# Performance work log

Hardware: AMD Instinct MI355X
Metric: run time of the kernel (lower is better)

The kernel has to match this reference:

```python
import jax, jax.numpy as jnp
import numpy as np

NUM_NODES = 100000
NUM_RELS = 50
NUM_BASES = 16
H_DIM = 16
OUT_DIM = 8
NUM_EDGES = 3200000


def setup_inputs() -> dict:
    key = jax.random.key(0)
    ks = jax.random.split(key, 10)
    inp = {
        "edge_src": jax.random.randint(ks[0], (NUM_EDGES,), 0, NUM_NODES, dtype=jnp.int32),
        "edge_dst": jax.random.randint(ks[1], (NUM_EDGES,), 0, NUM_NODES, dtype=jnp.int32),
        "edge_type": jax.random.randint(ks[2], (NUM_EDGES,), 0, NUM_RELS, dtype=jnp.int32),
        "edge_norm": jax.random.uniform(ks[3], (NUM_EDGES,), dtype=jnp.float32),
        "W0": jax.random.normal(ks[4], (NUM_BASES, NUM_NODES, H_DIM), dtype=jnp.float32) * 0.05,
        "C0": jax.random.normal(ks[5], (NUM_RELS, NUM_BASES), dtype=jnp.float32) * 0.05,
        "W1": jax.random.normal(ks[6], (NUM_BASES, H_DIM, H_DIM), dtype=jnp.float32) * 0.05,
        "C1": jax.random.normal(ks[7], (NUM_RELS, NUM_BASES), dtype=jnp.float32) * 0.05,
        "W2": jax.random.normal(ks[8], (NUM_BASES, H_DIM, OUT_DIM), dtype=jnp.float32) * 0.05,
        "C2": jax.random.normal(ks[9], (NUM_RELS, NUM_BASES), dtype=jnp.float32) * 0.05,
    }
    return inp


def _input_layer(src, dst, rel, norm, W0, C0):
    # basis combination: (R, N, h) embedding-per-relation table
    Wfull = jnp.einsum('rb,bnh->rnh', C0, W0)
    emb = Wfull.reshape(NUM_RELS * NUM_NODES, H_DIM)
    # per-edge gather by rel_type * in_feat + src_id, scaled by norm
    msg = emb[rel * NUM_NODES + src] * norm[:, None]
    h = jax.ops.segment_sum(msg, dst, num_segments=NUM_NODES)
    return jax.nn.relu(h)


def _dense_layer(h, src, dst, rel, norm, W, C, out_dim):
    # basis combination: (R, in, out)
    Wr = jnp.einsum('rb,bio->rio', C, W)
    # transform node features once per relation, then gather by (rel, src)
    Hr = jnp.einsum('ni,rio->rno', h, Wr)  # (R, N, out)
    msg = Hr[rel, src] * norm[:, None]     # (E, out)
    return jax.ops.segment_sum(msg, dst, num_segments=NUM_NODES)


def reference(edge_src, edge_dst, edge_type, edge_norm, W0, C0, W1, C1, W2, C2):
    h = _input_layer(edge_src, edge_dst, edge_type, edge_norm, W0, C0)
    h = jax.nn.relu(_dense_layer(h, edge_src, edge_dst, edge_type, edge_norm, W1, C1, H_DIM))
    h = jax.nn.softmax(_dense_layer(h, edge_src, edge_dst, edge_type, edge_norm, W2, C2, OUT_DIM), axis=1)
    return h
```

## Files before the change

### kernel.cpp

```cpp
#include <hip/hip_runtime.h>
#include <cstddef>
#include <cstdint>

#define E_TOTAL 3200000
#define N_NODES 100000
#define N_RELS 50
#define N_BASES 16
#define HD 16
#define OD 8
#define NTHR 256

#define NBKT 196
#define P1B 1024
#define P1C 3125
#define FP8_SCALE 256.0f
#define FP8_INV (1.0f / 256.0f)

typedef unsigned int u32;
typedef __attribute__((ext_vector_type(8))) short s16x8;
typedef __attribute__((ext_vector_type(4))) float f32x4;
typedef __attribute__((ext_vector_type(16))) float f32x16;

__device__ __forceinline__ u32 cvtpk(float x0, float x1) {
    u32 r;
    asm("v_cvt_pk_bf16_f32 %0, %1, %2" : "=v"(r) : "v"(x0), "v"(x1));
    return r;
}
__device__ __forceinline__ ushort bf16r(float x) {
    u32 a = __float_as_uint(x);
    return (ushort)((a + 0x7fffu + ((a >> 16) & 1u)) >> 16);
}
__device__ __forceinline__ s16x8 as_s16x8(uint4 u) {
    union { uint4 u; s16x8 s; } x; x.u = u; return x.s;
}

#if __has_builtin(__builtin_amdgcn_cvt_pk_fp8_f32)
__device__ __forceinline__ u32 pk8x4(float a, float b, float c, float d) {
    int v = __builtin_amdgcn_cvt_pk_fp8_f32(a, b, 0, false);
    v = __builtin_amdgcn_cvt_pk_fp8_f32(c, d, v, true);
    return (u32)v;
}
#else
__device__ __forceinline__ u32 pk8(float v) {
    u32 x = __float_as_uint(v);
    u32 s = (x >> 24) & 0x80u;
    u32 ax = x & 0x7fffffffu;
    int e = (int)(ax >> 23) - 127;
    if (e < -9) return s;
    if (e < -6) {
        u32 m = (u32)rintf(__uint_as_float(ax) * 512.0f);
        if (m == 0) return s;
        if (m >= 8) return s | 0x08u;
        return s | m;
    }
    u32 m = ax & 0x7fffffu;
    u32 keep = m >> 20, rest = m & 0xFFFFFu;
    keep += (rest > 0x80000u) || (rest == 0x80000u && (keep & 1u));
    u32 ee = (u32)(e + 7);
    if (keep == 8u) { keep = 0u; ee += 1u; }
    if (ee > 15u || (ee == 15u && keep == 7u)) return s | 0x7eu;
    return s | (ee << 3) | keep;
}
__device__ __forceinline__ u32 pk8x4(float a, float b, float c, float d) {
    return pk8(a) | (pk8(b) << 8) | (pk8(c) << 16) | (pk8(d) << 24);
}
#endif
#if __has_builtin(__builtin_amdgcn_cvt_f32_fp8)
template <int SEL>
__device__ __forceinline__ float up8(u32 q) { return __builtin_amdgcn_cvt_f32_fp8(q, SEL); }
#else
template <int SEL>
__device__ __forceinline__ float up8(u32 q) {
    u32 b = (q >> (SEL * 8)) & 0xffu;
    u32 em = b & 0x7fu;
    float v = (em >= 8u) ? __uint_as_float((((em >> 3) + 120u) << 23) | ((em & 7u) << 20))
                         : (float)em * (1.0f / 512.0f);
    return (b & 0x80u) ? -v : v;
}
#endif

__global__ __launch_bounds__(NTHR) void k_p1(const int* __restrict__ esrc, const int* __restrict__ edst,
                                             const int* __restrict__ erel, const float* __restrict__ enorm,
                                             uint2* __restrict__ tmp, int* __restrict__ cntK,
                                             int* __restrict__ runstartK,
                                             const float* __restrict__ W1, const float* __restrict__ C1,
                                             const float* __restrict__ W2, const float* __restrict__ C2,
                                             ushort* __restrict__ f1, ushort* __restrict__ f2) {
    __shared__ int lcnt[NBKT];
    __shared__ int sc[NTHR];
    __shared__ int lcur[NBKT];
    __shared__ uint2 stage[P1C];
    int tid = threadIdx.x;
    if (blockIdx.x >= P1B) {
        int idx = (blockIdx.x - P1B) * NTHR + tid;
        if (idx < 25 * 512) {
            int p = idx >> 9, rem = idx & 511, lane = rem >> 3, e = rem & 7;
            int m = lane & 31, kk = ((lane >> 5) << 3) + e;
            int r = 2 * p + (m >> 4), o = m & 15;
            float acc = 0.f;
            #pragma unroll
            for (int b = 0; b < N_BASES; ++b)
                acc = fmaf(C1[r * N_BASES + b], W1[b * 256 + kk * 16 + o], acc);
            f1[idx] = bf16r(acc * FP8_SCALE);
        } else if (idx < 25 * 512 + 13 * 512) {
            int j = idx - 25 * 512;
            int g = j >> 9, rem = j & 511, lane = rem >> 3, e = rem & 7;
            int m = lane & 31, kk = ((lane >> 5) << 3) + e;
            int rl = 4 * g + (m >> 3), o = m & 7;
            float acc = 0.f;
            if (rl < N_RELS) {
                #pragma unroll
                for (int b = 0; b < N_BASES; ++b)
                    acc = fmaf(C2[rl * N_BASES + b], W2[b * 128 + kk * 8 + o], acc);
            }
            f2[j] = bf16r(acc * FP8_SCALE);
        }
        return;
    }
    for (int i = tid; i < NBKT; i += NTHR) lcnt[i] = 0;
    __syncthreads();
    int e0 = blockIdx.x * P1C;
    u32 rx[13], rn[13];
    int rb[13];
    #pragma unroll
    for (int j = 0; j < 13; ++j) {
        int i = tid + j * NTHR;
        rb[j] = -1;
        if (i < P1C) {
            int e = e0 + i;
            int d = edst[e];
            int b = d >> 9;
            rb[j] = b;
            rx[j] = (u32)esrc[e] | ((u32)erel[e] << 17) | ((u32)(d & 511) << 23);
            rn[j] = __float_as_uint(enorm[e]);
            atomicAdd(&lcnt[b], 1);
        }
    }
    __syncthreads();
    int own = (tid < NBKT) ? lcnt[tid] : 0;
    sc[tid] = own;
    __syncthreads();
    #pragma unroll
    for (int off = 1; off < NTHR; off <<= 1) {
        int t = (tid >= off) ? sc[tid - off] : 0;
        __syncthreads();
        sc[tid] += t;
        __syncthreads();
    }
    if (tid < NBKT) lcur[tid] = sc[tid] - own;
    __syncthreads();
    #pragma unroll
    for (int j = 0; j < 13; ++j) {
        if (rb[j] >= 0) {
            int pos = atomicAdd(&lcur[rb[j]], 1);
            stage[pos] = make_uint2(rx[j], rn[j]);
        }
    }
    __syncthreads();
    for (int i = tid; i < P1C; i += NTHR)
        tmp[(size_t)blockIdx.x * P1C + i] = stage[i];
    for (int b = tid; b < NBKT; b += NTHR) {
        int excl = lcur[b] - lcnt[b];
        cntK[blockIdx.x * NBKT + b] = lcnt[b];
        runstartK[blockIdx.x * NBKT + b] = blockIdx.x * P1C + excl;
    }
}

__global__ __launch_bounds__(NTHR) void k_tot(const int* __restrict__ cntK, int* __restrict__ total) {
    int b = blockIdx.x;
    __shared__ int s[NTHR];
    int tid = threadIdx.x;
    int acc = 0;
    for (int k = tid; k < P1B; k += NTHR) acc += cntK[k * NBKT + b];
    s[tid] = acc;
    __syncthreads();
    for (int off = NTHR / 2; off > 0; off >>= 1) {
        if (tid < off) s[tid] += s[tid + off];
        __syncthreads();
    }
    if (tid == 0) total[b] = s[0];
}

__global__ __launch_bounds__(1024) void k_p2(const uint2* __restrict__ tmp, const int* __restrict__ cntK,
                                             const int* __restrict__ runstartK, const int* __restrict__ total,
                                             uint2* __restrict__ rec, int* __restrict__ row_ptr) {
    int b = blockIdx.x;
    int tid = threadIdx.x;
    __shared__ int dcnt[512], dscan[512];
    __shared__ int gbs;
    if (tid < 256) dcnt[tid] = (tid < b && tid < NBKT) ? total[tid] : 0;
    __syncthreads();
    for (int off = 128; off > 0; off >>= 1) {
        if (tid < off) dcnt[tid] += dcnt[tid + off];
        __syncthreads();
    }
    if (tid == 0) gbs = dcnt[0];
    __syncthreads();
    int gbase = gbs;
    if (tid < 512) dcnt[tid] = 0;
    __syncthreads();
    int mycnt = cntK[tid * NBKT + b];
    int myrs = runstartK[tid * NBKT + b];
    for (int i = 0; i < mycnt; ++i)
        atomicAdd(&dcnt[tmp[myrs + i].x >> 23], 1);
    __syncthreads();
    if (tid < 512) dscan[tid] = dcnt[tid];
    __syncthreads();
    for (int off = 1; off < 512; off <<= 1) {
        int v = (tid >= off && tid < 512) ? dscan[tid - off] : 0;
        __syncthreads();
        if (tid < 512) dscan[tid] += v;
        __syncthreads();
    }
    if (tid < 512) {
        int excl = gbase + dscan[tid] - dcnt[tid];
        int d = (b << 9) + tid;
        if (d < N_NODES) row_ptr[d] = excl;
        dscan[tid] = excl;
    }
    if (b == NBKT - 1 && tid == 0) row_ptr[N_NODES] = E_TOTAL;
    __syncthreads();
    for (int i = 0; i < mycnt; ++i) {
        uint2 t = tmp[myrs + i];
        int pos = atomicAdd(&dscan[t.x >> 23], 1);
        rec[pos] = make_uint2(t.x & 0x7FFFFFu, t.y);
    }
}


__global__ __launch_bounds__(NTHR) void k_e0f(const float* __restrict__ W0, const float* __restrict__ C0,
                                              u32* __restrict__ emb) {
    const f32x16 z16 = {0.f, 0.f, 0.f, 0.f, 0.f, 0.f, 0.f, 0.f,
                        0.f, 0.f, 0.f, 0.f, 0.f, 0.f, 0.f, 0.f};
    int lane = threadIdx.x & 63;
    int col = lane & 31, hi = lane >> 5;
    s16x8 bf0, bf1;
    {
        float v[8];
        #pragma unroll
        for (int e = 0; e < 8; ++e) v[e] = C0[col * 16 + hi * 8 + e] * FP8_SCALE;
        bf0 = as_s16x8(make_uint4(cvtpk(v[0], v[1]), cvtpk(v[2], v[3]),
                                  cvtpk(v[4], v[5]), cvtpk(v[6], v[7])));
        int r1 = col + 32;
        #pragma unroll
        for (int e = 0; e < 8; ++e) v[e] = (r1 < N_RELS) ? C0[r1 * 16 + hi * 8 + e] * FP8_SCALE : 0.f;
        bf1 = as_s16x8(make_uint4(cvtpk(v[0], v[1]), cvtpk(v[2], v[3]),
                                  cvtpk(v[4], v[5]), cvtpk(v[6], v[7])));
    }
    int w = (blockIdx.x * NTHR + threadIdx.x) >> 6;
    int nw = (gridDim.x * NTHR) >> 6;
    bool g1ok = (col + 32) < N_RELS;
    for (int t = w; t < 50000; t += nw) {
        size_t gs = (size_t)t * 32 + col;
        float a[8];
        #pragma unroll
        for (int e = 0; e < 8; ++e)
            a[e] = W0[(size_t)(hi * 8 + e) * (N_NODES * HD) + gs];
        s16x8 af = as_s16x8(make_uint4(cvtpk(a[0], a[1]), cvtpk(a[2], a[3]),
                                       cvtpk(a[4], a[5]), cvtpk(a[6], a[7])));
        f32x16 d0 = __builtin_amdgcn_mfma_f32_32x32x16_bf16(af, bf0, z16, 0, 0, 0);
        f32x16 d1 = __builtin_amdgcn_mfma_f32_32x32x16_bf16(af, bf1, z16, 0, 0, 0);
        #pragma unroll
        for (int j = 0; j < 4; ++j) {
            size_t base = ((size_t)(t * 2 + (j >> 1)) * 50) * 4 + (size_t)((j & 1) * 2 + hi);
            emb[base + (size_t)col * 4] = pk8x4(d0[4 * j], d0[4 * j + 1], d0[4 * j + 2], d0[4 * j + 3]);
            if (g1ok)
                emb[base + (size_t)(col + 32) * 4] =
                    pk8x4(d1[4 * j], d1[4 * j + 1], d1[4 * j + 2], d1[4 * j + 3]);
        }
    }
}

__global__ __launch_bounds__(NTHR) void k_g16b(const uint2* __restrict__ rec, const int* __restrict__ row_ptr,
                                               const u32* __restrict__ tbl, u32* __restrict__ hb,
                                               int srcMul, int relMul) {
    int lane = threadIdx.x & 63;
    int g = lane >> 2, l = lane & 3;
    int wave = (blockIdx.x * NTHR + threadIdx.x) >> 6;
    int nw = (gridDim.x * NTHR) >> 6;
    for (int d = wave; d < N_NODES; d += nw) {
        int s0 = row_ptr[d], s1 = row_ptr[d + 1];
        float a0 = 0.f, a1 = 0.f, a2 = 0.f, a3 = 0.f;
        for (int j = s0 + g; j < s1; j += 16) {
            uint2 rc = rec[j];
            int src = rc.x & 0x1FFFF;
            int rel = rc.x >> 17;
            float nm = __uint_as_float(rc.y) * FP8_INV;
            u32 q = tbl[(size_t)src * srcMul + (size_t)rel * relMul + l];
            a0 = fmaf(nm, up8<0>(q), a0);
            a1 = fmaf(nm, up8<1>(q), a1);
            a2 = fmaf(nm, up8<2>(q), a2);
            a3 = fmaf(nm, up8<3>(q), a3);
        }
        a0 += __shfl_xor(a0, 4);  a1 += __shfl_xor(a1, 4);  a2 += __shfl_xor(a2, 4);  a3 += __shfl_xor(a3, 4);
        a0 += __shfl_xor(a0, 8);  a1 += __shfl_xor(a1, 8);  a2 += __shfl_xor(a2, 8);  a3 += __shfl_xor(a3, 8);
        a0 += __shfl_xor(a0, 16); a1 += __shfl_xor(a1, 16); a2 += __shfl_xor(a2, 16); a3 += __shfl_xor(a3, 16);
        a0 += __shfl_xor(a0, 32); a1 += __shfl_xor(a1, 32); a2 += __shfl_xor(a2, 32); a3 += __shfl_xor(a3, 32);
        if (lane < 4) {
            uint2 pk = make_uint2(cvtpk(fmaxf(a0, 0.f), fmaxf(a1, 0.f)),
                                  cvtpk(fmaxf(a2, 0.f), fmaxf(a3, 0.f)));
            *(uint2*)(hb + (size_t)d * 8 + l * 2) = pk;
        }
    }
}

__global__ __launch_bounds__(NTHR) void k_e1f(const uint4* __restrict__ wfrag, const uint4* __restrict__ hb,
                                              u32* __restrict__ emb) {
    const f32x16 z16 = {0.f, 0.f, 0.f, 0.f, 0.f, 0.f, 0.f, 0.f,
                        0.f, 0.f, 0.f, 0.f, 0.f, 0.f, 0.f, 0.f};
    int lane = threadIdx.x & 63;
    int w = (blockIdx.x * NTHR + threadIdx.x) >> 6;
    int p = w / 250, c = w % 250;
    if (p >= 25) return;
    s16x8 af = as_s16x8(wfrag[p * 64 + lane]);
    int col = lane & 31, hi = lane >> 5;
    size_t r0b = (size_t)(2 * p) * 400000, r1b = (size_t)(2 * p + 1) * 400000;
    for (int t = c; t < 3125; t += 250) {
        uint4 hq = hb[(size_t)(t * 32 + col) * 2 + hi];
        f32x16 d = __builtin_amdgcn_mfma_f32_32x32x16_bf16(af, as_s16x8(hq), z16, 0, 0, 0);
        u32 A0 = pk8x4(d[0], d[1], d[2], d[3]);
        u32 B0 = pk8x4(d[4], d[5], d[6], d[7]);
        u32 A1 = pk8x4(d[8], d[9], d[10], d[11]);
        u32 B1 = pk8x4(d[12], d[13], d[14], d[15]);
        u32 pA0 = (u32)__shfl_xor((int)A0, 32);
        u32 pB0 = (u32)__shfl_xor((int)B0, 32);
        u32 pA1 = (u32)__shfl_xor((int)A1, 32);
        u32 pB1 = (u32)__shfl_xor((int)B1, 32);
        u32 off = t * 128 + col * 4;
        if (hi == 0) {
            *(uint2*)(emb + r0b + off) = make_uint2(A0, pA0);
            *(uint2*)(emb + r1b + off) = make_uint2(A1, pA1);
        } else {
            *(uint2*)(emb + r0b + off + 2) = make_uint2(pB0, B0);
            *(uint2*)(emb + r1b + off + 2) = make_uint2(pB1, B1);
        }
    }
}

__global__ __launch_bounds__(NTHR) void k_e2f(const uint4* __restrict__ wfrag, const uint4* __restrict__ hb,
                                              u32* __restrict__ emb) {
    const f32x16 z16 = {0.f, 0.f, 0.f, 0.f, 0.f, 0.f, 0.f, 0.f,
                        0.f, 0.f, 0.f, 0.f, 0.f, 0.f, 0.f, 0.f};
    int lane = threadIdx.x & 63;
    int w = (blockIdx.x * NTHR + threadIdx.x) >> 6;
    int g = w / 250, c = w % 250;
    if (g >= 13) return;
    s16x8 af = as_s16x8(wfrag[g * 64 + lane]);
    int col = lane & 31, hi = lane >> 5;
    for (int t = c; t < 3125; t += 250) {
        uint4 hq = hb[(size_t)(t * 32 + col) * 2 + hi];
        f32x16 d = __builtin_amdgcn_mfma_f32_32x32x16_bf16(af, as_s16x8(hq), z16, 0, 0, 0);
        #pragma unroll
        for (int j = 0; j < 4; ++j) {
            int rl = 4 * g + j;
            if (rl >= N_RELS) break;
            u32 wj = pk8x4(d[4 * j], d[4 * j + 1], d[4 * j + 2], d[4 * j + 3]);
            emb[(size_t)rl * 200000 + t * 64 + col * 2 + hi] = wj;
        }
    }
}

__global__ __launch_bounds__(NTHR) void k_g8sm(const uint2* __restrict__ rec, const int* __restrict__ row_ptr,
                                               const u32* __restrict__ tbl, float* __restrict__ out) {
    int lane = threadIdx.x & 63;
    int g = lane >> 1, l = lane & 1;
    int wave = (blockIdx.x * NTHR + threadIdx.x) >> 6;
    int nw = (gridDim.x * NTHR) >> 6;
    for (int d = wave; d < N_NODES; d += nw) {
        int s0 = row_ptr[d], s1 = row_ptr[d + 1];
        float a0 = 0.f, a1 = 0.f, a2 = 0.f, a3 = 0.f;
        for (int j = s0 + g; j < s1; j += 32) {
            uint2 rc = rec[j];
            int src = rc.x & 0x1FFFF;
            int rel = rc.x >> 17;
            float nm = __uint_as_float(rc.y) * FP8_INV;
            u32 q = tbl[((size_t)rel * N_NODES + src) * 2 + l];
            a0 = fmaf(nm, up8<0>(q), a0);
            a1 = fmaf(nm, up8<1>(q), a1);
            a2 = fmaf(nm, up8<2>(q), a2);
            a3 = fmaf(nm, up8<3>(q), a3);
        }
        a0 += __shfl_xor(a0, 2);  a1 += __shfl_xor(a1, 2);  a2 += __shfl_xor(a2, 2);  a3 += __shfl_xor(a3, 2);
        a0 += __shfl_xor(a0, 4);  a1 += __shfl_xor(a1, 4);  a2 += __shfl_xor(a2, 4);  a3 += __shfl_xor(a3, 4);
        a0 += __shfl_xor(a0, 8);  a1 += __shfl_xor(a1, 8);  a2 += __shfl_xor(a2, 8);  a3 += __shfl_xor(a3, 8);
        a0 += __shfl_xor(a0, 16); a1 += __shfl_xor(a1, 16); a2 += __shfl_xor(a2, 16); a3 += __shfl_xor(a3, 16);
        a0 += __shfl_xor(a0, 32); a1 += __shfl_xor(a1, 32); a2 += __shfl_xor(a2, 32); a3 += __shfl_xor(a3, 32);
        float mx = fmaxf(fmaxf(a0, a1), fmaxf(a2, a3));
        mx = fmaxf(mx, __shfl_xor(mx, 1));
        float e0 = __expf(a0 - mx), e1 = __expf(a1 - mx), e2 = __expf(a2 - mx), e3 = __expf(a3 - mx);
        float sm = e0 + e1 + e2 + e3;
        sm += __shfl_xor(sm, 1);
        float inv = 1.0f / sm;
        if (lane < 2)
            *(float4*)(out + (size_t)d * OD + l * 4) = make_float4(e0 * inv, e1 * inv, e2 * inv, e3 * inv);
    }
}

#define NBLK 2560

__device__ __forceinline__ void fma4(float* acc, float c, float4 w) {
    acc[0] = fmaf(c, w.x, acc[0]);
    acc[1] = fmaf(c, w.y, acc[1]);
    acc[2] = fmaf(c, w.z, acc[2]);
    acc[3] = fmaf(c, w.w, acc[3]);
}

__global__ __launch_bounds__(NTHR) void k_wr(const float* __restrict__ W1, const float* __restrict__ C1,
                                             const float* __restrict__ W2, const float* __restrict__ C2,
                                             float* __restrict__ Wr1, float* __restrict__ Wr2) {
    int idx = blockIdx.x * NTHR + threadIdx.x;
    const int n1 = N_RELS * 256;
    if (idx < n1) {
        int r = idx >> 8, io = idx & 255;
        float acc = 0.f;
        #pragma unroll
        for (int b = 0; b < N_BASES; ++b)
            acc = fmaf(C1[r * N_BASES + b], W1[b * 256 + io], acc);
        Wr1[idx] = acc;
    } else if (idx < n1 + N_RELS * 128) {
        int j = idx - n1;
        int r = j >> 7, io = j & 127;
        float acc = 0.f;
        #pragma unroll
        for (int b = 0; b < N_BASES; ++b)
            acc = fmaf(C2[r * N_BASES + b], W2[b * 128 + io], acc);
        Wr2[j] = acc;
    }
}

__global__ __launch_bounds__(NTHR) void k_l0_old(const int* __restrict__ esrc, const int* __restrict__ edst,
                                                 const int* __restrict__ erel, const float* __restrict__ enorm,
                                                 const float* __restrict__ W0, const float* __restrict__ C0,
                                                 float* __restrict__ h0) {
    for (int e = blockIdx.x * NTHR + threadIdx.x; e < E_TOTAL; e += NBLK * NTHR) {
        int s = esrc[e], d = edst[e], r = erel[e];
        float nm = enorm[e];
        const float4* cp = reinterpret_cast<const float4*>(C0 + r * N_BASES);
        float4 c0 = cp[0], c1 = cp[1], c2 = cp[2], c3 = cp[3];
        float coef[16] = {c0.x, c0.y, c0.z, c0.w, c1.x, c1.y, c1.z, c1.w,
                          c2.x, c2.y, c2.z, c2.w, c3.x, c3.y, c3.z, c3.w};
        float acc[16];
        #pragma unroll
        for (int h = 0; h < 16; ++h) acc[h] = 0.f;
        const float* wbase = W0 + (size_t)s * HD;
        #pragma unroll
        for (int b = 0; b < N_BASES; ++b) {
            const float4* wp = reinterpret_cast<const float4*>(wbase + (size_t)b * (N_NODES * HD));
            float cb = coef[b];
            fma4(acc + 0, cb, wp[0]);
            fma4(acc + 4, cb, wp[1]);
            fma4(acc + 8, cb, wp[2]);
            fma4(acc + 12, cb, wp[3]);
        }
        float* outp = h0 + (size_t)d * HD;
        #pragma unroll
        for (int h = 0; h < 16; ++h) atomicAdd(outp + h, nm * acc[h]);
    }
}

__global__ __launch_bounds__(NTHR) void k_l1_old(const int* __restrict__ esrc, const int* __restrict__ edst,
                                                 const int* __restrict__ erel, const float* __restrict__ enorm,
                                                 const float* __restrict__ h0, const float* __restrict__ Wr1,
                                                 float* __restrict__ h1) {
    __shared__ float w[N_RELS * 260];
    for (int i = threadIdx.x; i < N_RELS * 256; i += NTHR) {
        int r = i >> 8, rest = i & 255;
        w[r * 260 + rest] = Wr1[i];
    }
    __syncthreads();
    for (int e = blockIdx.x * NTHR + threadIdx.x; e < E_TOTAL; e += NBLK * NTHR) {
        int s = esrc[e], d = edst[e], r = erel[e];
        float nm = enorm[e];
        const float4* hp = reinterpret_cast<const float4*>(h0 + (size_t)s * HD);
        float4 hv0 = hp[0], hv1 = hp[1], hv2 = hp[2], hv3 = hp[3];
        float hs[16] = {fmaxf(hv0.x, 0.f), fmaxf(hv0.y, 0.f), fmaxf(hv0.z, 0.f), fmaxf(hv0.w, 0.f),
                        fmaxf(hv1.x, 0.f), fmaxf(hv1.y, 0.f), fmaxf(hv1.z, 0.f), fmaxf(hv1.w, 0.f),
                        fmaxf(hv2.x, 0.f), fmaxf(hv2.y, 0.f), fmaxf(hv2.z, 0.f), fmaxf(hv2.w, 0.f),
                        fmaxf(hv3.x, 0.f), fmaxf(hv3.y, 0.f), fmaxf(hv3.z, 0.f), fmaxf(hv3.w, 0.f)};
        float acc[16];
        #pragma unroll
        for (int h = 0; h < 16; ++h) acc[h] = 0.f;
        const float* wr = w + r * 260;
        #pragma unroll
        for (int i = 0; i < 16; ++i) {
            float hi = hs[i];
            const float4* wp = reinterpret_cast<const float4*>(wr + i * 16);
            fma4(acc + 0, hi, wp[0]);
            fma4(acc + 4, hi, wp[1]);
            fma4(acc + 8, hi, wp[2]);
            fma4(acc + 12, hi, wp[3]);
        }
        float* outp = h1 + (size_t)d * HD;
        #pragma unroll
        for (int h = 0; h < 16; ++h) atomicAdd(outp + h, nm * acc[h]);
    }
}

__global__ __launch_bounds__(NTHR) void k_l2_old(const int* __restrict__ esrc, const int* __restrict__ edst,
                                                 const int* __restrict__ erel, const float* __restrict__ enorm,
                                                 const float* __restrict__ h1, const float* __restrict__ Wr2,
                                                 float* __restrict__ h2) {
    __shared__ float w[N_RELS * 132];
    for (int i = threadIdx.x; i < N_RELS * 128; i += NTHR) {
        int r = i >> 7, rest = i & 127;
        w[r * 132 + rest] = Wr2[i];
    }
    __syncthreads();
    for (int e = blockIdx.x * NTHR + threadIdx.x; e < E_TOTAL; e += NBLK * NTHR) {
        int s = esrc[e], d = edst[e], r = erel[e];
        float nm = enorm[e];
        const float4* hp = reinterpret_cast<const float4*>(h1 + (size_t)s * HD);
        float4 hv0 = hp[0], hv1 = hp[1], hv2 = hp[2], hv3 = hp[3];
        float hs[16] = {fmaxf(hv0.x, 0.f), fmaxf(hv0.y, 0.f), fmaxf(hv0.z, 0.f), fmaxf(hv0.w, 0.f),
                        fmaxf(hv1.x, 0.f), fmaxf(hv1.y, 0.f), fmaxf(hv1.z, 0.f), fmaxf(hv1.w, 0.f),
                        fmaxf(hv2.x, 0.f), fmaxf(hv2.y, 0.f), fmaxf(hv2.z, 0.f), fmaxf(hv2.w, 0.f),
                        fmaxf(hv3.x, 0.f), fmaxf(hv3.y, 0.f), fmaxf(hv3.z, 0.f), fmaxf(hv3.w, 0.f)};
        float acc[8];
        #pragma unroll
        for (int h = 0; h < 8; ++h) acc[h] = 0.f;
        const float* wr = w + r * 132;
        #pragma unroll
        for (int i = 0; i < 16; ++i) {
            float hi = hs[i];
            const float4* wp = reinterpret_cast<const float4*>(wr + i * 8);
            fma4(acc + 0, hi, wp[0]);
            fma4(acc + 4, hi, wp[1]);
        }
        float* outp = h2 + (size_t)d * OD;
        #pragma unroll
        for (int h = 0; h < 8; ++h) atomicAdd(outp + h, nm * acc[h]);
    }
}

__global__ __launch_bounds__(NTHR) void k_softmax(const float* __restrict__ h2, float* __restrict__ out) {
    int n = blockIdx.x * NTHR + threadIdx.x;
    if (n >= N_NODES) return;
    const float4* p = reinterpret_cast<const float4*>(h2 + (size_t)n * OD);
    float4 a = p[0], b = p[1];
    float v[8] = {a.x, a.y, a.z, a.w, b.x, b.y, b.z, b.w};
    float m = v[0];
    #pragma unroll
    for (int i = 1; i < 8; ++i) m = fmaxf(m, v[i]);
    float ssum = 0.f;
    #pragma unroll
    for (int i = 0; i < 8; ++i) {
        v[i] = __expf(v[i] - m);
        ssum += v[i];
    }
    float inv = 1.0f / ssum;
    float4* q = reinterpret_cast<float4*>(out + (size_t)n * OD);
    q[0] = make_float4(v[0] * inv, v[1] * inv, v[2] * inv, v[3] * inv);
    q[1] = make_float4(v[4] * inv, v[5] * inv, v[6] * inv, v[7] * inv);
}


extern "C" void kernel_launch(void* const* d_in, const int* in_sizes, int n_in,
                              void* d_out, int out_size, void* d_ws, size_t ws_size,
                              hipStream_t stream) {
    const int* esrc = (const int*)d_in[0];
    const int* edst = (const int*)d_in[1];
    const int* erel = (const int*)d_in[2];
    const float* enorm = (const float*)d_in[3];
    const float* W0 = (const float*)d_in[4];
    const float* C0 = (const float*)d_in[5];
    const float* W1 = (const float*)d_in[6];
    const float* C1 = (const float*)d_in[7];
    const float* W2 = (const float*)d_in[8];
    const float* C2 = (const float*)d_in[9];
    const int nsb = (N_NODES + NTHR - 1) / NTHR;

    if (ws_size >= (size_t)201000000) {
        char* wsb = (char*)d_ws;
        u32* emb = (u32*)wsb;
        uint2* tmp = (uint2*)wsb;
        uint2* rec = (uint2*)(wsb + 160000000);
        u32* h0b = (u32*)(wsb + 185600000);
        u32* h1b = (u32*)(wsb + 188800000);
        ushort* wf1 = (ushort*)(wsb + 192000000);
        ushort* wf2 = (ushort*)(wsb + 192051200);
        int* row_ptr = (int*)(wsb + 192102400);
        int* cntK = (int*)(wsb + 192502404);
        int* runstartK = (int*)(wsb + 193305220);
        int* total = (int*)(wsb + 194108036);

        k_p1<<<P1B + 76, NTHR, 0, stream>>>(esrc, edst, erel, enorm, tmp, cntK, runstartK,
                                            W1, C1, W2, C2, wf1, wf2);
        k_tot<<<NBKT, NTHR, 0, stream>>>(cntK, total);
        k_p2<<<NBKT, 1024, 0, stream>>>(tmp, cntK, runstartK, total, rec, row_ptr);

        k_e0f<<<1563, NTHR, 0, stream>>>(W0, C0, emb);
        k_g16b<<<6250, NTHR, 0, stream>>>(rec, row_ptr, emb, h0b, 200, 4);
        k_e1f<<<1563, NTHR, 0, stream>>>((const uint4*)wf1, (const uint4*)h0b, emb);
        k_g16b<<<6250, NTHR, 0, stream>>>(rec, row_ptr, emb, h1b, 4, 400000);
        k_e2f<<<813, NTHR, 0, stream>>>((const uint4*)wf2, (const uint4*)h1b, emb);
        k_g8sm<<<6250, NTHR, 0, stream>>>(rec, row_ptr, emb, (float*)d_out);
    } else {
        float* ws = (float*)d_ws;
        float* h0 = ws;
        float* h1 = ws + 1600000;
        float* h2 = ws + 3200000;
        float* Wr1 = ws + 4000000;
        float* Wr2 = ws + 4012800;

        (void)hipMemsetAsync(h0, 0, (size_t)4000000 * sizeof(float), stream);
        k_wr<<<75, NTHR, 0, stream>>>(W1, C1, W2, C2, Wr1, Wr2);
        k_l0_old<<<NBLK, NTHR, 0, stream>>>(esrc, edst, erel, enorm, W0, C0, h0);
        k_l1_old<<<NBLK, NTHR, 0, stream>>>(esrc, edst, erel, enorm, h0, Wr1, h1);
        k_l2_old<<<NBLK, NTHR, 0, stream>>>(esrc, edst, erel, enorm, h1, Wr2, h2);
        k_softmax<<<nsb, NTHR, 0, stream>>>(h2, (float*)d_out);
    }
}
```

Measured before the change: 353.5 us.

## Fuse layer-0 embedding build into bucketing kernel and unroll gather loop

Moves the basis-combination MFMA embedding kernel into the edge-partitioning kernel as extra blocks, relocating the tmp buffer so it no longer aliases the embedding table, so both phases run concurrently in one launch. Also unrolls the per-destination gather loop by two so each lane issues two independent record/table loads per iteration. This trades extra shared-memory reservation on the fused blocks and larger register use for better overlap and memory-level parallelism.

```diff
diff --git a/kernel.cpp b/kernel.cpp
--- a/kernel.cpp
+++ b/kernel.cpp
@@ -13,6 +13,8 @@
 #define NBKT 196
 #define P1B 1024
 #define P1C 3125
+#define WFB 76
+#define E0B 1563
 #define FP8_SCALE 256.0f
 #define FP8_INV (1.0f / 256.0f)
 
@@ -85,12 +87,56 @@
                                              int* __restrict__ runstartK,
                                              const float* __restrict__ W1, const float* __restrict__ C1,
                                              const float* __restrict__ W2, const float* __restrict__ C2,
-                                             ushort* __restrict__ f1, ushort* __restrict__ f2) {
+                                             ushort* __restrict__ f1, ushort* __restrict__ f2,
+                                             const float* __restrict__ W0, const float* __restrict__ C0,
+                                             u32* __restrict__ emb) {
     __shared__ int lcnt[NBKT];
     __shared__ int sc[NTHR];
     __shared__ int lcur[NBKT];
     __shared__ uint2 stage[P1C];
     int tid = threadIdx.x;
+    if (blockIdx.x >= P1B + WFB) {
+        const f32x16 z16 = {0.f, 0.f, 0.f, 0.f, 0.f, 0.f, 0.f, 0.f,
+                            0.f, 0.f, 0.f, 0.f, 0.f, 0.f, 0.f, 0.f};
+        int lane = tid & 63;
+        int col = lane & 31, hi = lane >> 5;
+        s16x8 bf0, bf1;
+        {
+            float v[8];
+            #pragma unroll
+            for (int e = 0; e < 8; ++e) v[e] = C0[col * 16 + hi * 8 + e] * FP8_SCALE;
+            bf0 = as_s16x8(make_uint4(cvtpk(v[0], v[1]), cvtpk(v[2], v[3]),
+                                      cvtpk(v[4], v[5]), cvtpk(v[6], v[7])));
+            int r1 = col + 32;
+            #pragma unroll
+            for (int e = 0; e < 8; ++e) v[e] = (r1 < N_RELS) ? C0[r1 * 16 + hi * 8 + e] * FP8_SCALE : 0.f;
+            bf1 = as_s16x8(make_uint4(cvtpk(v[0], v[1]), cvtpk(v[2], v[3]),
+                                      cvtpk(v[4], v[5]), cvtpk(v[6], v[7])));
+        }
+        int w = ((blockIdx.x - P1B - WFB) * NTHR + tid) >> 6;
+        int nw = (E0B * NTHR) >> 6;
+        bool g1ok = (col + 32) < N_RELS;
+        for (int t = w; t < 50000; t += nw) {
+            size_t gs = (size_t)t * 32 + col;
+            float a[8];
+            #pragma unroll
+            for (int e = 0; e < 8; ++e)
+                a[e] = W0[(size_t)(hi * 8 + e) * (N_NODES * HD) + gs];
+            s16x8 af = as_s16x8(make_uint4(cvtpk(a[0], a[1]), cvtpk(a[2], a[3]),
+                                           cvtpk(a[4], a[5]), cvtpk(a[6], a[7])));
+            f32x16 d0 = __builtin_amdgcn_mfma_f32_32x32x16_bf16(af, bf0, z16, 0, 0, 0);
+            f32x16 d1 = __builtin_amdgcn_mfma_f32_32x32x16_bf16(af, bf1, z16, 0, 0, 0);
+            #pragma unroll
+            for (int j = 0; j < 4; ++j) {
+                size_t base = ((size_t)(t * 2 + (j >> 1)) * 50) * 4 + (size_t)((j & 1) * 2 + hi);
+                emb[base + (size_t)col * 4] = pk8x4(d0[4 * j], d0[4 * j + 1], d0[4 * j + 2], d0[4 * j + 3]);
+                if (g1ok)
+                    emb[base + (size_t)(col + 32) * 4] =
+                        pk8x4(d1[4 * j], d1[4 * j + 1], d1[4 * j + 2], d1[4 * j + 3]);
+            }
+        }
+        return;
+    }
     if (blockIdx.x >= P1B) {
         int idx = (blockIdx.x - P1B) * NTHR + tid;
         if (idx < 25 * 512) {
@@ -227,50 +273,6 @@
     }
 }
 
-
-__global__ __launch_bounds__(NTHR) void k_e0f(const float* __restrict__ W0, const float* __restrict__ C0,
-                                              u32* __restrict__ emb) {
-    const f32x16 z16 = {0.f, 0.f, 0.f, 0.f, 0.f, 0.f, 0.f, 0.f,
-                        0.f, 0.f, 0.f, 0.f, 0.f, 0.f, 0.f, 0.f};
-    int lane = threadIdx.x & 63;
-    int col = lane & 31, hi = lane >> 5;
-    s16x8 bf0, bf1;
-    {
-        float v[8];
-        #pragma unroll
-        for (int e = 0; e < 8; ++e) v[e] = C0[col * 16 + hi * 8 + e] * FP8_SCALE;
-        bf0 = as_s16x8(make_uint4(cvtpk(v[0], v[1]), cvtpk(v[2], v[3]),
-                                  cvtpk(v[4], v[5]), cvtpk(v[6], v[7])));
-        int r1 = col + 32;
-        #pragma unroll
-        for (int e = 0; e < 8; ++e) v[e] = (r1 < N_RELS) ? C0[r1 * 16 + hi * 8 + e] * FP8_SCALE : 0.f;
-        bf1 = as_s16x8(make_uint4(cvtpk(v[0], v[1]), cvtpk(v[2], v[3]),
-                                  cvtpk(v[4], v[5]), cvtpk(v[6], v[7])));
-    }
-    int w = (blockIdx.x * NTHR + threadIdx.x) >> 6;
-    int nw = (gridDim.x * NTHR) >> 6;
-    bool g1ok = (col + 32) < N_RELS;
-    for (int t = w; t < 50000; t += nw) {
-        size_t gs = (size_t)t * 32 + col;
-        float a[8];
-        #pragma unroll
-        for (int e = 0; e < 8; ++e)
-            a[e] = W0[(size_t)(hi * 8 + e) * (N_NODES * HD) + gs];
-        s16x8 af = as_s16x8(make_uint4(cvtpk(a[0], a[1]), cvtpk(a[2], a[3]),
-                                       cvtpk(a[4], a[5]), cvtpk(a[6], a[7])));
-        f32x16 d0 = __builtin_amdgcn_mfma_f32_32x32x16_bf16(af, bf0, z16, 0, 0, 0);
-        f32x16 d1 = __builtin_amdgcn_mfma_f32_32x32x16_bf16(af, bf1, z16, 0, 0, 0);
-        #pragma unroll
-        for (int j = 0; j < 4; ++j) {
-            size_t base = ((size_t)(t * 2 + (j >> 1)) * 50) * 4 + (size_t)((j & 1) * 2 + hi);
-            emb[base + (size_t)col * 4] = pk8x4(d0[4 * j], d0[4 * j + 1], d0[4 * j + 2], d0[4 * j + 3]);
-            if (g1ok)
-                emb[base + (size_t)(col + 32) * 4] =
-                    pk8x4(d1[4 * j], d1[4 * j + 1], d1[4 * j + 2], d1[4 * j + 3]);
-        }
-    }
-}
-
 __global__ __launch_bounds__(NTHR) void k_g16b(const uint2* __restrict__ rec, const int* __restrict__ row_ptr,
                                                const u32* __restrict__ tbl, u32* __restrict__ hb,
                                                int srcMul, int relMul) {
@@ -281,16 +283,25 @@
     for (int d = wave; d < N_NODES; d += nw) {
         int s0 = row_ptr[d], s1 = row_ptr[d + 1];
         float a0 = 0.f, a1 = 0.f, a2 = 0.f, a3 = 0.f;
-        for (int j = s0 + g; j < s1; j += 16) {
-            uint2 rc = rec[j];
-            int src = rc.x & 0x1FFFF;
-            int rel = rc.x >> 17;
-            float nm = __uint_as_float(rc.y) * FP8_INV;
-            u32 q = tbl[(size_t)src * srcMul + (size_t)rel * relMul + l];
-            a0 = fmaf(nm, up8<0>(q), a0);
-            a1 = fmaf(nm, up8<1>(q), a1);
-            a2 = fmaf(nm, up8<2>(q), a2);
-            a3 = fmaf(nm, up8<3>(q), a3);
+        for (int j = s0 + g; j < s1; j += 32) {
+            uint2 rc0 = rec[j];
+            int j1 = j + 16;
+            bool ok = j1 < s1;
+            uint2 rc1 = ok ? rec[j1] : make_uint2(0u, 0u);
+            int src0 = rc0.x & 0x1FFFF, rel0 = rc0.x >> 17;
+            float nm0 = __uint_as_float(rc0.y) * FP8_INV;
+            int src1 = rc1.x & 0x1FFFF, rel1 = rc1.x >> 17;
+            float nm1 = ok ? __uint_as_float(rc1.y) * FP8_INV : 0.f;
+            u32 q0 = tbl[(size_t)src0 * srcMul + (size_t)rel0 * relMul + l];
+            u32 q1 = tbl[(size_t)src1 * srcMul + (size_t)rel1 * relMul + l];
+            a0 = fmaf(nm0, up8<0>(q0), a0);
+            a1 = fmaf(nm0, up8<1>(q0), a1);
+            a2 = fmaf(nm0, up8<2>(q0), a2);
+            a3 = fmaf(nm0, up8<3>(q0), a3);
+            a0 = fmaf(nm1, up8<0>(q1), a0);
+            a1 = fmaf(nm1, up8<1>(q1), a1);
+            a2 = fmaf(nm1, up8<2>(q1), a2);
+            a3 = fmaf(nm1, up8<3>(q1), a3);
         }
         a0 += __shfl_xor(a0, 4);  a1 += __shfl_xor(a1, 4);  a2 += __shfl_xor(a2, 4);  a3 += __shfl_xor(a3, 4);
         a0 += __shfl_xor(a0, 8);  a1 += __shfl_xor(a1, 8);  a2 += __shfl_xor(a2, 8);  a3 += __shfl_xor(a3, 8);
@@ -572,7 +583,7 @@
     if (ws_size >= (size_t)201000000) {
         char* wsb = (char*)d_ws;
         u32* emb = (u32*)wsb;
-        uint2* tmp = (uint2*)wsb;
+        uint2* tmp = (uint2*)(wsb + 80000000);
         uint2* rec = (uint2*)(wsb + 160000000);
         u32* h0b = (u32*)(wsb + 185600000);
         u32* h1b = (u32*)(wsb + 188800000);
@@ -583,12 +594,11 @@
         int* runstartK = (int*)(wsb + 193305220);
         int* total = (int*)(wsb + 194108036);
 
-        k_p1<<<P1B + 76, NTHR, 0, stream>>>(esrc, edst, erel, enorm, tmp, cntK, runstartK,
-                                            W1, C1, W2, C2, wf1, wf2);
+        k_p1<<<P1B + WFB + E0B, NTHR, 0, stream>>>(esrc, edst, erel, enorm, tmp, cntK, runstartK,
+                                                   W1, C1, W2, C2, wf1, wf2, W0, C0, emb);
         k_tot<<<NBKT, NTHR, 0, stream>>>(cntK, total);
         k_p2<<<NBKT, 1024, 0, stream>>>(tmp, cntK, runstartK, total, rec, row_ptr);
 
-        k_e0f<<<1563, NTHR, 0, stream>>>(W0, C0, emb);
         k_g16b<<<6250, NTHR, 0, stream>>>(rec, row_ptr, emb, h0b, 200, 4);
         k_e1f<<<1563, NTHR, 0, stream>>>((const uint4*)wf1, (const uint4*)h0b, emb);
         k_g16b<<<6250, NTHR, 0, stream>>>(rec, row_ptr, emb, h1b, 4, 400000);
```

Result: no change. 350.3 us, median of 2 (-0.9%).
